# Kernel optimization log

Hardware: AMD Instinct MI355X
Metric: run time of the kernel (lower is better)

Reference implementation:

```python
import jax, jax.numpy as jnp
import numpy as np

NPOINT = 1024
NSAMPLE = 32


def _fps(xyz, npoint):
    # farthest point sampling; xyz: (B, N, 3) -> idx (B, npoint) int32
    B, N, _ = xyz.shape

    def step(carry, _):
        dist, far = carry
        centroid = jnp.take_along_axis(xyz, far[:, None, None], axis=1)  # (B,1,3)
        d = jnp.sum((xyz - centroid) ** 2, axis=-1)  # (B,N)
        dist = jnp.minimum(dist, d)
        nxt = jnp.argmax(dist, axis=1).astype(jnp.int32)
        return (dist, nxt), far

    init = (jnp.full((B, N), 1e10, xyz.dtype), jnp.zeros((B,), jnp.int32))
    _, idx = jax.lax.scan(step, init, None, length=npoint)
    return idx.T  # (B, npoint)


def _forward(xyz, features, afa_w1, afa_b1, afa_w2, afa_b2, afa_ww, afa_bw,
             mlp_w1, mlp_b1, mlp_w2, mlp_b2, mlp_w3, mlp_b3):
    B, N, _ = xyz.shape
    M = NSAMPLE
    # --- furthest point sampling + gather new_xyz ---
    fps_idx = _fps(xyz, NPOINT)                                   # (B, Np)
    new_xyz = jnp.take_along_axis(xyz, fps_idx[..., None], axis=1)  # (B, Np, 3)
    # --- kNN grouping (QueryAndGroup with use_xyz) ---
    sqd = (jnp.sum(new_xyz ** 2, -1)[..., None]
           + jnp.sum(xyz ** 2, -1)[:, None, :]
           - 2.0 * jnp.einsum('bpd,bnd->bpn', new_xyz, xyz))       # (B, Np, N)
    _, knn = jax.lax.top_k(-sqd, M)                               # (B, Np, M)
    gather = jax.vmap(lambda a, i: a[i])
    gxyz = gather(xyz, knn) - new_xyz[:, :, None, :]              # (B, Np, M, 3)
    gfeat = gather(features.transpose(0, 2, 1), knn)              # (B, Np, M, Cin)
    x = jnp.concatenate([gxyz, gfeat], axis=-1).transpose(0, 3, 1, 2)  # (B, C, Np, M)
    # --- AFA: pairwise diff + eye self term ---
    eye = jnp.eye(M, dtype=x.dtype)
    pair = x[..., :, None] - x[..., None, :] + x[..., :, None] * eye  # (B, C, Np, M, M)
    conv5 = lambda w, b, t: jnp.einsum('oc,bcnij->bonij', w, t) + b[None, :, None, None, None]
    h = jax.nn.relu(conv5(afa_w1, afa_b1, pair))
    h = jax.nn.relu(conv5(afa_w2, afa_b2, h))
    wgt = conv5(afa_ww, afa_bw, h)                                 # (B, C, Np, M, M)
    afa = jnp.sum(pair * wgt, axis=-1)                             # (B, C, Np, M)
    nf = x + afa
    # --- shared MLP (1x1 convs, relu, no bn) + max pool over M ---
    conv4 = lambda w, b, t: jnp.einsum('oc,bcnm->bonm', w, t) + b[None, :, None, None]
    h = jax.nn.relu(conv4(mlp_w1, mlp_b1, nf))
    h = jax.nn.relu(conv4(mlp_w2, mlp_b2, h))
    h = jax.nn.relu(conv4(mlp_w3, mlp_b3, h))
    out = jnp.max(h, axis=-1)                                      # (B, 128, Np)
    return new_xyz, out


def setup_inputs() -> dict:
    key = jax.random.key(0)
    ks = jax.random.split(key, 10)
    B, N, Cin = 2, 4096, 32
    C = Cin + 3  # use_xyz adds 3 -> 35

    def w(k, o, i):
        return (jax.random.normal(k, (o, i), jnp.float32) / np.float32(np.sqrt(i)))

    return {
        'xyz': jax.random.uniform(ks[0], (B, N, 3), jnp.float32),
        'features': jax.random.normal(ks[1], (B, Cin, N), jnp.float32),
        'afa_w1': w(ks[2], 16, C), 'afa_b1': jnp.zeros((16,), jnp.float32),
        'afa_w2': w(ks[3], 16, 16), 'afa_b2': jnp.zeros((16,), jnp.float32),
        'afa_ww': w(ks[4], C, 16), 'afa_bw': jnp.zeros((C,), jnp.float32),
        'mlp_w1': w(ks[5], 64, C), 'mlp_b1': jnp.zeros((64,), jnp.float32),
        'mlp_w2': w(ks[6], 64, 64), 'mlp_b2': jnp.zeros((64,), jnp.float32),
        'mlp_w3': w(ks[7], 128, 64), 'mlp_b3': jnp.zeros((128,), jnp.float32),
    }


def reference(xyz, features, afa_w1, afa_b1, afa_w2, afa_b2, afa_ww, afa_bw,
              mlp_w1, mlp_b1, mlp_w2, mlp_b2, mlp_w3, mlp_b3):
    return _forward(xyz, features, afa_w1, afa_b1, afa_w2, afa_b2, afa_ww, afa_bw,
                    mlp_w1, mlp_b1, mlp_w2, mlp_b2, mlp_w3, mlp_b3)
```

## Files before the change

### kernel.cpp

```cpp
#include <hip/hip_runtime.h>

#define BB 2
#define NN 4096
#define NP 1024
#define MM 32
#define CC 35
#define CIN 32

#define KEY_DPP(CTRL) do { \
    int _lo = (int)(unsigned)key, _hi = (int)(unsigned)(key >> 32); \
    int _olo = __builtin_amdgcn_mov_dpp(_lo, CTRL, 0xF, 0xF, true); \
    int _ohi = __builtin_amdgcn_mov_dpp(_hi, CTRL, 0xF, 0xF, true); \
    unsigned long long _ok = ((unsigned long long)(unsigned)_ohi << 32) | (unsigned)_olo; \
    if (_ok > key) key = _ok; \
} while (0)

__launch_bounds__(256)
__global__ void fps_prep_kernel(const float* __restrict__ xyz, float* __restrict__ newxyz_out,
                                const float* __restrict__ w1, const float* __restrict__ w2,
                                const float* __restrict__ w3,
                                float* __restrict__ w1T, float* __restrict__ w2T,
                                float* __restrict__ w3T)
{
#pragma clang fp contract(off)
    const int t = threadIdx.x;

    if (blockIdx.x >= BB) {
        int g = (blockIdx.x - BB) * 256 + t;
        int stride = 8 * 256;
        for (int i = g; i < 64 * CC; i += stride) { int o = i / CC, c = i % CC; w1T[c * 64 + o] = w1[i]; }
        for (int i = g; i < 64 * 64; i += stride) { int o = i >> 6, c = i & 63; w2T[c * 64 + o] = w2[i]; }
        for (int i = g; i < 128 * 64; i += stride) { int o = i >> 6, c = i & 63; w3T[c * 128 + o] = w3[i]; }
        return;
    }

    const int b = blockIdx.x;
    const float* xb = xyz + b * NN * 3;

    __shared__ float4 pc[NN];
    __shared__ float nxs[NP * 3];
    __shared__ unsigned long long red[2][16];

    float px[16], py[16], pz[16], dist[16];
#pragma unroll
    for (int k = 0; k < 16; ++k) {
        int n = t + 256 * k;
        float x = xb[n * 3 + 0];
        float y = xb[n * 3 + 1];
        float z = xb[n * 3 + 2];
        px[k] = x; py[k] = y; pz[k] = z;
        dist[k] = 1e10f;
        pc[n] = make_float4(x, y, z, 0.0f);
    }
    __syncthreads();

    int far = 0;
    for (int s = 0; s < NP; ++s) {
        float4 c = pc[far];
        if (t == 0) {
            nxs[s * 3 + 0] = c.x;
            nxs[s * 3 + 1] = c.y;
            nxs[s * 3 + 2] = c.z;
        }
        const float cx = c.x, cy = c.y, cz = c.z;

        float bv = -1.0f; int bi = 0;
#pragma unroll
        for (int k = 0; k < 16; ++k) {
            float dx = px[k] - cx, dy = py[k] - cy, dz = pz[k] - cz;
            float d = (dx * dx + dy * dy) + dz * dz;
            float dd = fminf(dist[k], d);
            dist[k] = dd;
            if (dd > bv) { bv = dd; bi = t + 256 * k; }
        }

        unsigned long long key =
            ((unsigned long long)(unsigned)__float_as_int(bv) << 32)
            | (unsigned)(0xFFFFFFFFu - (unsigned)bi);

        KEY_DPP(0xB1);
        KEY_DPP(0x4E);
        KEY_DPP(0x141);
        KEY_DPP(0x140);

        const int buf = s & 1;
        if ((t & 15) == 0) red[buf][t >> 4] = key;
        __syncthreads();

        key = red[buf][t & 15];
        KEY_DPP(0xB1);
        KEY_DPP(0x4E);
        KEY_DPP(0x141);
        KEY_DPP(0x140);
        far = (int)(0xFFFFFFFFu - (unsigned)key);
    }

    __syncthreads();
#pragma unroll
    for (int j = 0; j < 12; ++j) {
        int i = t + 256 * j;
        newxyz_out[b * NP * 3 + i] = nxs[i];
    }
}

__launch_bounds__(256)
__global__ void knn_kernel(const float* __restrict__ xyz, const float* __restrict__ newxyz,
                           int* __restrict__ knn_out)
{
#pragma clang fp contract(off)
    const int bp = blockIdx.x;
    const int b = bp >> 10;
    const int t = threadIdx.x;
    const float* xb = xyz + b * NN * 3;

    const float qx = newxyz[bp * 3 + 0];
    const float qy = newxyz[bp * 3 + 1];
    const float qz = newxyz[bp * 3 + 2];
    const float qn = (qx * qx + qy * qy) + qz * qz;

    __shared__ float dist[NN];
    __shared__ float redV[4];
    __shared__ int   redI[4];

#pragma unroll
    for (int k = 0; k < 16; ++k) {
        int n = t + 256 * k;
        float x = xb[n * 3 + 0], y = xb[n * 3 + 1], z = xb[n * 3 + 2];
        float xn = (x * x + y * y) + z * z;
        float dt = (qx * x + qy * y) + qz * z;
        dist[n] = (qn + xn) - 2.0f * dt;
    }
    __syncthreads();

    for (int r = 0; r < MM; ++r) {
        float bv = 1e30f; int bi = NN;
#pragma unroll
        for (int k = 0; k < 16; ++k) {
            int n = t + 256 * k;
            float v = dist[n];
            if (v < bv) { bv = v; bi = n; }
        }
#pragma unroll
        for (int off = 1; off < 64; off <<= 1) {
            float ov = __shfl_xor(bv, off);
            int   oi = __shfl_xor(bi, off);
            if (ov < bv || (ov == bv && oi < bi)) { bv = ov; bi = oi; }
        }
        if ((t & 63) == 0) { redV[t >> 6] = bv; redI[t >> 6] = bi; }
        __syncthreads();
        bv = redV[0]; bi = redI[0];
#pragma unroll
        for (int w = 1; w < 4; ++w) {
            float ov = redV[w]; int oi = redI[w];
            if (ov < bv || (ov == bv && oi < bi)) { bv = ov; bi = oi; }
        }
        if (t == 0) { knn_out[bp * MM + r] = bi; dist[bi] = 1e30f; }
        __syncthreads();
    }
}

__launch_bounds__(256)
__global__ void afa_mlp_kernel(const float* __restrict__ xyz, const float* __restrict__ feat,
                               const float* __restrict__ newxyz, const int* __restrict__ knn,
                               const float* __restrict__ aw1, const float* __restrict__ ab1,
                               const float* __restrict__ aw2, const float* __restrict__ ab2,
                               const float* __restrict__ aww, const float* __restrict__ abw,
                               const float* __restrict__ w1T, const float* __restrict__ b1,
                               const float* __restrict__ w2T, const float* __restrict__ b2,
                               const float* __restrict__ w3T, const float* __restrict__ b3,
                               float* __restrict__ out)
{
    const int bp = blockIdx.x;
    const int b = bp >> 10, p = bp & 1023;
    const int t = threadIdx.x;

    __shared__ int   idxs[MM];
    __shared__ float xs_t[MM][36];
    __shared__ float u_lds[MM][20];
    __shared__ float nfs[CC][MM];
    __shared__ float h1s[64][36];
    __shared__ float h2s[64][36];
    __shared__ float pmax[128][2];

    if (t < MM) idxs[t] = knn[bp * MM + t];
    __syncthreads();

    {
        const int m = t & 31, c0 = t >> 5;
        const int id = idxs[m] & (NN - 1);
        for (int c = c0; c < CC; c += 8) {
            float v;
            if (c < 3) v = xyz[(b * NN + id) * 3 + c] - newxyz[bp * 3 + c];
            else       v = feat[(b * CIN + (c - 3)) * NN + id];
            xs_t[m][c] = v;
        }
        if (c0 == 0) xs_t[m][35] = 0.0f;
    }
    __syncthreads();

    const int i = t >> 3, jg = t & 7;

    float xi[36];
    {
        const float4* xp = (const float4*)&xs_t[i][0];
#pragma unroll
        for (int q = 0; q < 9; ++q) {
            float4 v = xp[q];
            xi[4 * q] = v.x; xi[4 * q + 1] = v.y; xi[4 * q + 2] = v.z; xi[4 * q + 3] = v.w;
        }
    }

    float u16[16];
#pragma unroll
    for (int o = 0; o < 16; ++o) {
        float acc = 0.0f;
#pragma unroll
        for (int c = 0; c < CC; ++c) acc += aw1[o * CC + c] * xi[c];
        u16[o] = acc;
    }
    if (jg == 0) {
        float4* up = (float4*)&u_lds[i][0];
#pragma unroll
        for (int q = 0; q < 4; ++q)
            up[q] = make_float4(u16[4 * q], u16[4 * q + 1], u16[4 * q + 2], u16[4 * q + 3]);
    }
    __syncthreads();

    float afa[CC];
#pragma unroll
    for (int c = 0; c < CC; ++c) afa[c] = 0.0f;

#pragma unroll
    for (int jk = 0; jk < 4; ++jk) {
        const int j = jg + 8 * jk;
        const bool diag = (i == j);

        float uj[16];
        {
            const float4* up = (const float4*)&u_lds[j][0];
#pragma unroll
            for (int q = 0; q < 4; ++q) {
                float4 v = up[q];
                uj[4 * q] = v.x; uj[4 * q + 1] = v.y; uj[4 * q + 2] = v.z; uj[4 * q + 3] = v.w;
            }
        }

        float h1[16];
#pragma unroll
        for (int o = 0; o < 16; ++o) {
            float s = u16[o] - uj[o];
            if (diag) s += u16[o];
            h1[o] = fmaxf(s + ab1[o], 0.0f);
        }

        float xj[36];
        {
            const float4* xp = (const float4*)&xs_t[j][0];
#pragma unroll
            for (int q = 0; q < 9; ++q) {
                float4 v = xp[q];
                xj[4 * q] = v.x; xj[4 * q + 1] = v.y; xj[4 * q + 2] = v.z; xj[4 * q + 3] = v.w;
            }
        }

        float h2[16];
#pragma unroll
        for (int o = 0; o < 16; ++o) {
            float acc = ab2[o];
#pragma unroll
            for (int c = 0; c < 16; ++c) acc += aw2[o * 16 + c] * h1[c];
            h2[o] = fmaxf(acc, 0.0f);
        }

#pragma unroll
        for (int c = 0; c < CC; ++c) {
            float acc = abw[c];
#pragma unroll
            for (int k = 0; k < 16; ++k) acc += aww[c * 16 + k] * h2[k];
            float pc_ = xi[c] - xj[c];
            if (diag) pc_ += xi[c];
            afa[c] += pc_ * acc;
        }
    }

#pragma unroll
    for (int c = 0; c < CC; ++c) {
        float v = afa[c];
        v += __shfl_xor(v, 1);
        v += __shfl_xor(v, 2);
        v += __shfl_xor(v, 4);
        if (jg == 0) nfs[c][i] = xi[c] + v;
    }
    __syncthreads();

    {
        const int o = t & 63, ib = (t >> 6) << 3;
        float acc[8];
        float bb = b1[o];
#pragma unroll
        for (int k = 0; k < 8; ++k) acc[k] = bb;
        for (int c = 0; c < CC; ++c) {
            float w = w1T[c * 64 + o];
            const float4* np4 = (const float4*)&nfs[c][ib];
            float4 n0 = np4[0], n1 = np4[1];
            acc[0] += w * n0.x; acc[1] += w * n0.y; acc[2] += w * n0.z; acc[3] += w * n0.w;
            acc[4] += w * n1.x; acc[5] += w * n1.y; acc[6] += w * n1.z; acc[7] += w * n1.w;
        }
        float4 r0 = { fmaxf(acc[0], 0.0f), fmaxf(acc[1], 0.0f), fmaxf(acc[2], 0.0f), fmaxf(acc[3], 0.0f) };
        float4 r1 = { fmaxf(acc[4], 0.0f), fmaxf(acc[5], 0.0f), fmaxf(acc[6], 0.0f), fmaxf(acc[7], 0.0f) };
        *(float4*)&h1s[o][ib]     = r0;
        *(float4*)&h1s[o][ib + 4] = r1;
    }
    __syncthreads();

    {
        const int o = t & 63, ib = (t >> 6) << 3;
        float acc[8];
        float bb = b2[o];
#pragma unroll
        for (int k = 0; k < 8; ++k) acc[k] = bb;
        for (int c = 0; c < 64; ++c) {
            float w = w2T[c * 64 + o];
            const float4* hp4 = (const float4*)&h1s[c][ib];
            float4 h0 = hp4[0], h1v = hp4[1];
            acc[0] += w * h0.x; acc[1] += w * h0.y; acc[2] += w * h0.z; acc[3] += w * h0.w;
            acc[4] += w * h1v.x; acc[5] += w * h1v.y; acc[6] += w * h1v.z; acc[7] += w * h1v.w;
        }
        float4 r0 = { fmaxf(acc[0], 0.0f), fmaxf(acc[1], 0.0f), fmaxf(acc[2], 0.0f), fmaxf(acc[3], 0.0f) };
        float4 r1 = { fmaxf(acc[4], 0.0f), fmaxf(acc[5], 0.0f), fmaxf(acc[6], 0.0f), fmaxf(acc[7], 0.0f) };
        *(float4*)&h2s[o][ib]     = r0;
        *(float4*)&h2s[o][ib + 4] = r1;
    }
    __syncthreads();

    {
        const int o = t & 127, ib = (t >> 7) << 4;
        float acc[16];
        float bb = b3[o];
#pragma unroll
        for (int k = 0; k < 16; ++k) acc[k] = bb;
        for (int c = 0; c < 64; ++c) {
            float w = w3T[c * 128 + o];
            const float4* hp4 = (const float4*)&h2s[c][ib];
            float4 h0 = hp4[0], h1v = hp4[1], h2v = hp4[2], h3v = hp4[3];
            acc[0]  += w * h0.x;  acc[1]  += w * h0.y;  acc[2]  += w * h0.z;  acc[3]  += w * h0.w;
            acc[4]  += w * h1v.x; acc[5]  += w * h1v.y; acc[6]  += w * h1v.z; acc[7]  += w * h1v.w;
            acc[8]  += w * h2v.x; acc[9]  += w * h2v.y; acc[10] += w * h2v.z; acc[11] += w * h2v.w;
            acc[12] += w * h3v.x; acc[13] += w * h3v.y; acc[14] += w * h3v.z; acc[15] += w * h3v.w;
        }
        float mx = -1e30f;
#pragma unroll
        for (int k = 0; k < 16; ++k) mx = fmaxf(mx, fmaxf(acc[k], 0.0f));
        pmax[o][t >> 7] = mx;
    }
    __syncthreads();

    if (t < 128) {
        float v = fmaxf(pmax[t][0], pmax[t][1]);
        out[(b * 128 + t) * NP + p] = v;
    }
}

extern "C" void kernel_launch(void* const* d_in, const int* in_sizes, int n_in,
                              void* d_out, int out_size, void* d_ws, size_t ws_size,
                              hipStream_t stream)
{
    const float* xyz  = (const float*)d_in[0];
    const float* feat = (const float*)d_in[1];
    const float* aw1  = (const float*)d_in[2];
    const float* ab1  = (const float*)d_in[3];
    const float* aw2  = (const float*)d_in[4];
    const float* ab2  = (const float*)d_in[5];
    const float* aww  = (const float*)d_in[6];
    const float* abw  = (const float*)d_in[7];
    const float* mw1  = (const float*)d_in[8];
    const float* mb1  = (const float*)d_in[9];
    const float* mw2  = (const float*)d_in[10];
    const float* mb2  = (const float*)d_in[11];
    const float* mw3  = (const float*)d_in[12];
    const float* mb3  = (const float*)d_in[13];

    float* out    = (float*)d_out;
    float* newxyz = out;
    float* out2   = out + BB * NP * 3;

    int*   knn = (int*)d_ws;
    float* w1T = (float*)((char*)d_ws + (1 << 19));
    float* w2T = w1T + CC * 64;
    float* w3T = w2T + 64 * 64;

    fps_prep_kernel<<<dim3(BB + 8), dim3(256), 0, stream>>>(xyz, newxyz,
                                                            mw1, mw2, mw3, w1T, w2T, w3T);
    knn_kernel<<<dim3(BB * NP), dim3(256), 0, stream>>>(xyz, newxyz, knn);
    afa_mlp_kernel<<<dim3(BB * NP), dim3(256), 0, stream>>>(
        xyz, feat, newxyz, knn,
        aw1, ab1, aw2, ab2, aww, abw,
        w1T, mb1, w2T, mb2, w3T, mb3, out2);
}
```

Baseline: 813.2 us.

## Spatially bin points in FPS and skip lanes whose cluster cannot change

The farthest-point-sampling kernel now runs with 512 threads and counting-sorts the points into an 8x8x8 grid. Each thread therefore owns 8 spatially adjacent points, and it keeps a bounding sphere (centroid and radius) around them. Each iteration, a lane can skip the distance update when the new centroid is too far away to lower its current max distance. If every lane in a wavefront can skip, the whole wavefront skips the inner loop. The idea is to cut the per-iteration arithmetic of the serial 1024-step loop, at the cost of a sort preamble and a two-stage 32-entry reduction. The cell computation assumes coordinates lie in [0,1).

After: 937.3 us. 1.15x slower.

```diff
diff --git a/kernel.cpp b/kernel.cpp
--- a/kernel.cpp
+++ b/kernel.cpp
@@ -15,7 +15,7 @@
     if (_ok > key) key = _ok; \
 } while (0)
 
-__launch_bounds__(256)
+__launch_bounds__(512)
 __global__ void fps_prep_kernel(const float* __restrict__ xyz, float* __restrict__ newxyz_out,
                                 const float* __restrict__ w1, const float* __restrict__ w2,
                                 const float* __restrict__ w3,
@@ -26,8 +26,8 @@
     const int t = threadIdx.x;
 
     if (blockIdx.x >= BB) {
-        int g = (blockIdx.x - BB) * 256 + t;
-        int stride = 8 * 256;
+        int g = (blockIdx.x - BB) * 512 + t;
+        int stride = 8 * 512;
         for (int i = g; i < 64 * CC; i += stride) { int o = i / CC, c = i % CC; w1T[c * 64 + o] = w1[i]; }
         for (int i = g; i < 64 * 64; i += stride) { int o = i >> 6, c = i & 63; w2T[c * 64 + o] = w2[i]; }
         for (int i = g; i < 128 * 64; i += stride) { int o = i >> 6, c = i & 63; w3T[c * 128 + o] = w3[i]; }
@@ -38,20 +38,86 @@
     const float* xb = xyz + b * NN * 3;
 
     __shared__ float4 pc[NN];
-    __shared__ float nxs[NP * 3];
-    __shared__ unsigned long long red[2][16];
-
-    float px[16], py[16], pz[16], dist[16];
-#pragma unroll
-    for (int k = 0; k < 16; ++k) {
-        int n = t + 256 * k;
+    __shared__ float  sxa[NN];
+    __shared__ float  sya[NN];
+    __shared__ float  sza[NN];
+    __shared__ int    sida[NN];
+    __shared__ int    cnt[512];
+    __shared__ int    wsum[8];
+    __shared__ unsigned long long red[2][32];
+    float* nxs = sxa;
+
+    float lx[8], ly[8], lz[8];
+    int   lcell[8];
+    cnt[t] = 0;
+    __syncthreads();
+#pragma unroll
+    for (int k = 0; k < 8; ++k) {
+        int n = t + 512 * k;
         float x = xb[n * 3 + 0];
         float y = xb[n * 3 + 1];
         float z = xb[n * 3 + 2];
-        px[k] = x; py[k] = y; pz[k] = z;
+        lx[k] = x; ly[k] = y; lz[k] = z;
+        pc[n] = make_float4(x, y, z, 0.0f);
+        int ix = min(7, (int)(x * 8.0f));
+        int iy = min(7, (int)(y * 8.0f));
+        int iz = min(7, (int)(z * 8.0f));
+        lcell[k] = (iz << 6) | (iy << 3) | ix;
+        atomicAdd(&cnt[lcell[k]], 1);
+    }
+    __syncthreads();
+
+    {
+        int c = cnt[t];
+        int incl = c;
+        const int lane = t & 63, w = t >> 6;
+#pragma unroll
+        for (int off = 1; off < 64; off <<= 1) {
+            int o = __shfl_up(incl, off);
+            if (lane >= off) incl += o;
+        }
+        if (lane == 63) wsum[w] = incl;
+        __syncthreads();
+        int base = 0;
+        for (int ww = 0; ww < 8; ++ww) if (ww < w) base += wsum[ww];
+        int excl = base + incl - c;
+        __syncthreads();
+        cnt[t] = excl;
+        __syncthreads();
+    }
+
+#pragma unroll
+    for (int k = 0; k < 8; ++k) {
+        int pos = atomicAdd(&cnt[lcell[k]], 1);
+        sxa[pos] = lx[k];
+        sya[pos] = ly[k];
+        sza[pos] = lz[k];
+        sida[pos] = t + 512 * k;
+    }
+    __syncthreads();
+
+    float px[8], py[8], pz[8], dist[8];
+    unsigned lowk[8];
+    float ctx = 0.0f, cty = 0.0f, ctz = 0.0f;
+#pragma unroll
+    for (int k = 0; k < 8; ++k) {
+        int pos = 8 * t + k;
+        px[k] = sxa[pos]; py[k] = sya[pos]; pz[k] = sza[pos];
+        lowk[k] = 0xFFFFFFFFu - (unsigned)sida[pos];
         dist[k] = 1e10f;
-        pc[n] = make_float4(x, y, z, 0.0f);
-    }
+        ctx += px[k]; cty += py[k]; ctz += pz[k];
+    }
+    ctx *= 0.125f; cty *= 0.125f; ctz *= 0.125f;
+    float r2m = 0.0f;
+#pragma unroll
+    for (int k = 0; k < 8; ++k) {
+        float dx = px[k] - ctx, dy = py[k] - cty, dz = pz[k] - ctz;
+        float d2 = (dx * dx + dy * dy) + dz * dz;
+        r2m = fmaxf(r2m, d2);
+    }
+    const float rr = sqrtf(r2m) * 1.0002f + 1e-7f;
+    unsigned long long bkey =
+        ((unsigned long long)(unsigned)__float_as_int(1e10f) << 32);
     __syncthreads();
 
     int far = 0;
@@ -64,20 +130,28 @@
         }
         const float cx = c.x, cy = c.y, cz = c.z;
 
-        float bv = -1.0f; int bi = 0;
-#pragma unroll
-        for (int k = 0; k < 16; ++k) {
-            float dx = px[k] - cx, dy = py[k] - cy, dz = pz[k] - cz;
-            float d = (dx * dx + dy * dy) + dz * dz;
-            float dd = fminf(dist[k], d);
-            dist[k] = dd;
-            if (dd > bv) { bv = dd; bi = t + 256 * k; }
-        }
-
-        unsigned long long key =
-            ((unsigned long long)(unsigned)__float_as_int(bv) << 32)
-            | (unsigned)(0xFFFFFFFFu - (unsigned)bi);
-
+        float dxc = ctx - cx, dyc = cty - cy, dzc = ctz - cz;
+        float d2c = (dxc * dxc + dyc * dyc) + dzc * dzc;
+        float m = sqrtf(d2c) - rr;
+        float bvf = __uint_as_float((unsigned)(bkey >> 32));
+        int lane_skip = (m > 0.0f) && (m * m > bvf * 1.0005f);
+
+        if (!__all(lane_skip)) {
+            unsigned long long nb = 0ull;
+#pragma unroll
+            for (int k = 0; k < 8; ++k) {
+                float dx = px[k] - cx, dy = py[k] - cy, dz = pz[k] - cz;
+                float d = (dx * dx + dy * dy) + dz * dz;
+                float dd = fminf(dist[k], d);
+                dist[k] = dd;
+                unsigned long long kk =
+                    ((unsigned long long)(unsigned)__float_as_int(dd) << 32) | lowk[k];
+                if (kk > nb) nb = kk;
+            }
+            bkey = nb;
+        }
+
+        unsigned long long key = bkey;
         KEY_DPP(0xB1);
         KEY_DPP(0x4E);
         KEY_DPP(0x141);
@@ -87,7 +161,11 @@
         if ((t & 15) == 0) red[buf][t >> 4] = key;
         __syncthreads();
 
-        key = red[buf][t & 15];
+        {
+            unsigned long long k0 = red[buf][t & 15];
+            unsigned long long k1 = red[buf][16 + (t & 15)];
+            key = (k1 > k0) ? k1 : k0;
+        }
         KEY_DPP(0xB1);
         KEY_DPP(0x4E);
         KEY_DPP(0x141);
@@ -97,8 +175,8 @@
 
     __syncthreads();
 #pragma unroll
-    for (int j = 0; j < 12; ++j) {
-        int i = t + 256 * j;
+    for (int j = 0; j < 6; ++j) {
+        int i = t + 512 * j;
         newxyz_out[b * NP * 3 + i] = nxs[i];
     }
 }
@@ -248,9 +326,9 @@
         float h1[16];
 #pragma unroll
         for (int o = 0; o < 16; ++o) {
-            float s = u16[o] - uj[o];
-            if (diag) s += u16[o];
-            h1[o] = fmaxf(s + ab1[o], 0.0f);
+            float sv = u16[o] - uj[o];
+            if (diag) sv += u16[o];
+            h1[o] = fmaxf(sv + ab1[o], 0.0f);
         }
 
         float xj[36];
@@ -389,7 +467,7 @@
     float* w2T = w1T + CC * 64;
     float* w3T = w2T + 64 * 64;
 
-    fps_prep_kernel<<<dim3(BB + 8), dim3(256), 0, stream>>>(xyz, newxyz,
+    fps_prep_kernel<<<dim3(BB + 8), dim3(512), 0, stream>>>(xyz, newxyz,
                                                             mw1, mw2, mw3, w1T, w2T, w3T);
     knn_kernel<<<dim3(BB * NP), dim3(256), 0, stream>>>(xyz, newxyz, knn);
     afa_mlp_kernel<<<dim3(BB * NP), dim3(256), 0, stream>>>(
```

## Replace iterative kNN argmin with radix histogram select and bucket ranking

Applied to the files above, without the earlier changes.

The kNN kernel no longer runs 32 rounds of block-wide argmin over 4096 distances. It maps each distance to an order-preserving unsigned key, builds a 256-bin histogram on the top byte, and finds the bucket that holds the 32nd element with a prefix scan. Elements below that bucket are written out directly, and the boundary bucket is ranked by pairwise comparison, with the old iterative path kept as a fallback if the bucket is large. This removes most of the per-round barriers and reductions, at the cost of LDS atomics. Output order within the first cntBelow slots becomes atomic-order rather than sorted, which could matter if downstream code depends on neighbour order.

New measurement: 769.4 us. 1.06x faster.

```diff
diff --git a/kernel.cpp b/kernel.cpp
--- a/kernel.cpp
+++ b/kernel.cpp
@@ -118,9 +118,15 @@
     const float qz = newxyz[bp * 3 + 2];
     const float qn = (qx * qx + qy * qy) + qz * qz;
 
-    __shared__ float dist[NN];
-    __shared__ float redV[4];
-    __shared__ int   redI[4];
+    __shared__ unsigned kxs[NN];
+    __shared__ int hist[256];
+    __shared__ int wsum[4];
+    __shared__ unsigned long long blist[512];
+    __shared__ int scal[4];
+
+    hist[t] = 0;
+    if (t < 4) scal[t] = 0;
+    __syncthreads();
 
 #pragma unroll
     for (int k = 0; k < 16; ++k) {
@@ -128,34 +134,87 @@
         float x = xb[n * 3 + 0], y = xb[n * 3 + 1], z = xb[n * 3 + 2];
         float xn = (x * x + y * y) + z * z;
         float dt = (qx * x + qy * y) + qz * z;
-        dist[n] = (qn + xn) - 2.0f * dt;
-    }
-    __syncthreads();
-
-    for (int r = 0; r < MM; ++r) {
-        float bv = 1e30f; int bi = NN;
-#pragma unroll
-        for (int k = 0; k < 16; ++k) {
-            int n = t + 256 * k;
-            float v = dist[n];
-            if (v < bv) { bv = v; bi = n; }
-        }
+        float d = (qn + xn) - 2.0f * dt;
+        unsigned bits = __float_as_uint(d);
+        unsigned kx = bits ^ ((unsigned)((int)bits >> 31) | 0x80000000u);
+        kxs[n] = kx;
+        atomicAdd(&hist[kx >> 24], 1);
+    }
+    __syncthreads();
+
+    {
+        int c = hist[t];
+        int incl = c;
+        const int lane = t & 63, w = t >> 6;
 #pragma unroll
         for (int off = 1; off < 64; off <<= 1) {
-            float ov = __shfl_xor(bv, off);
-            int   oi = __shfl_xor(bi, off);
-            if (ov < bv || (ov == bv && oi < bi)) { bv = ov; bi = oi; }
-        }
-        if ((t & 63) == 0) { redV[t >> 6] = bv; redI[t >> 6] = bi; }
+            int o = __shfl_up(incl, off);
+            if (lane >= off) incl += o;
+        }
+        if (lane == 63) wsum[w] = incl;
         __syncthreads();
-        bv = redV[0]; bi = redI[0];
-#pragma unroll
-        for (int w = 1; w < 4; ++w) {
-            float ov = redV[w]; int oi = redI[w];
-            if (ov < bv || (ov == bv && oi < bi)) { bv = ov; bi = oi; }
-        }
-        if (t == 0) { knn_out[bp * MM + r] = bi; dist[bi] = 1e30f; }
-        __syncthreads();
+        int base = 0;
+        for (int ww = 0; ww < 4; ++ww) if (ww < w) base += wsum[ww];
+        int excl = base + incl - c;
+        if (excl < MM && MM <= excl + c) { scal[0] = t; scal[1] = excl; }
+    }
+    __syncthreads();
+
+    const int B = scal[0];
+    const int cntBelow = scal[1];
+    const unsigned bstart = (unsigned)B << 24;
+
+#pragma unroll
+    for (int k = 0; k < 16; ++k) {
+        int n = t + 256 * k;
+        unsigned kx = kxs[n];
+        if (kx < bstart) {
+            int pos = atomicAdd(&scal[3], 1);
+            knn_out[bp * MM + pos] = n;
+        } else if ((kx >> 24) == (unsigned)B) {
+            int pos = atomicAdd(&scal[2], 1);
+            if (pos < 512) blist[pos] = ((unsigned long long)kx << 32) | (unsigned)n;
+        }
+    }
+    __syncthreads();
+
+    const int nB = scal[2];
+    const int k2 = MM - cntBelow;
+
+    if (nB <= 512) {
+        for (int m = t; m < nB; m += 256) {
+            unsigned long long my = blist[m];
+            int rank = 0;
+            for (int q = 0; q < nB; ++q) rank += (blist[q] < my) ? 1 : 0;
+            if (rank < k2)
+                knn_out[bp * MM + (cntBelow + rank)] = (int)(my & 0xFFFFFFFFu);
+        }
+    } else {
+        for (int r = 0; r < MM; ++r) {
+            unsigned bvk = 0xFFFFFFFFu; int bi = NN;
+#pragma unroll
+            for (int k = 0; k < 16; ++k) {
+                int n = t + 256 * k;
+                unsigned v = kxs[n];
+                if (v < bvk) { bvk = v; bi = n; }
+            }
+#pragma unroll
+            for (int off = 1; off < 64; off <<= 1) {
+                unsigned ov = __shfl_xor(bvk, off);
+                int   oi = __shfl_xor(bi, off);
+                if (ov < bvk || (ov == bvk && oi < bi)) { bvk = ov; bi = oi; }
+            }
+            if ((t & 63) == 0) { hist[t >> 6] = (int)bvk; wsum[t >> 6] = bi; }
+            __syncthreads();
+            unsigned fv = (unsigned)hist[0]; int fi = wsum[0];
+#pragma unroll
+            for (int w = 1; w < 4; ++w) {
+                unsigned ov = (unsigned)hist[w]; int oi = wsum[w];
+                if (ov < fv || (ov == fv && oi < fi)) { fv = ov; fi = oi; }
+            }
+            if (t == 0) { knn_out[bp * MM + r] = fi; kxs[fi] = 0xFFFFFFFFu; }
+            __syncthreads();
+        }
     }
 }
 
@@ -248,9 +307,9 @@
         float h1[16];
 #pragma unroll
         for (int o = 0; o < 16; ++o) {
-            float s = u16[o] - uj[o];
-            if (diag) s += u16[o];
-            h1[o] = fmaxf(s + ab1[o], 0.0f);
+            float sv = u16[o] - uj[o];
+            if (diag) sv += u16[o];
+            h1[o] = fmaxf(sv + ab1[o], 0.0f);
         }
 
         float xj[36];
```
